# Performance work log

Hardware: AMD Instinct MI355X
Metric: run time of the kernel (lower is better)

The kernel has to match this reference:

```python
import jax, jax.numpy as jnp
import numpy as np

B = 128          # batch
T = 196          # total_patches per view (2 views -> 2*T tokens)
ENC = 1024       # encoder_embed_dim
DEC = 512        # decoder_embed_dim
V = 98           # num unmasked (visible) tokens per sample
M = 2 * T - V    # num masked tokens (294)


def setup_inputs() -> dict:
    key = jax.random.key(0)
    kx, kperm, kw, kmt, kpos, kview = jax.random.split(key, 6)
    x = jax.random.normal(kx, (B, V, ENC), jnp.float32)
    # masked_ids: unique ids per row in [0, 2T) — built from permutations
    perms = jax.vmap(jax.random.permutation, in_axes=(0, None))(
        jax.random.split(kperm, B), 2 * T)
    masked_ids = perms[:, :M].astype(jnp.int64)
    W = jax.random.normal(kw, (DEC, ENC), jnp.float32) * 0.02
    b = jnp.zeros((DEC,), jnp.float32)
    mask_token = jax.random.normal(kmt, (1, 1, DEC), jnp.float32)
    pos_embed = jax.random.normal(kpos, (1, 2 * T, DEC), jnp.float32)
    view_embed = jax.random.normal(kview, (2, DEC), jnp.float32)
    return {"x": x, "masked_ids": masked_ids, "W": W, "b": b,
            "mask_token": mask_token, "pos_embed": pos_embed,
            "view_embed": view_embed}


def reference(x, masked_ids, W, b, mask_token, pos_embed, view_embed):
    Bn = x.shape[0]
    # Linear: enc -> dec
    xp = jnp.einsum('bve,de->bvd', x, W) + b          # (B, V, DEC)
    # visible ids = sorted complement of masked_ids (vectorized, no batch loop)
    rows = jnp.arange(Bn)[:, None]
    vis_mask = jnp.ones((Bn, 2 * T), bool).at[rows, masked_ids].set(False)
    # stable argsort puts True(visible, ~mask=False) positions first, in order
    visible_ids = jnp.argsort(~vis_mask, axis=1)[:, :V]  # (B, V)
    # scatter projected visible tokens into mask-token placeholders
    base = jnp.broadcast_to(mask_token, (Bn, 2 * T, DEC))
    view = base.at[rows, visible_ids].set(xp)          # (B, 2T, DEC)
    # per-view embedding: first T tokens -> view 0, last T -> view 1
    ve = jnp.concatenate([
        jnp.broadcast_to(view_embed[0], (T, DEC)),
        jnp.broadcast_to(view_embed[1], (T, DEC))], axis=0)  # (2T, DEC)
    return view + pos_embed + ve[None, :, :]
```

## Files before the change

### kernel.cpp

```cpp
#include <hip/hip_runtime.h>

#define BATCH 128
#define VIS   98
#define TOK   196
#define TOK2  392
#define ENC   1024
#define DEC   512
#define MSK   294

#define NWB 256

#define NGEMM 784
#define NFILL 1568

typedef __bf16 bf16x8 __attribute__((ext_vector_type(8)));
typedef float  f32x4  __attribute__((ext_vector_type(4)));

__device__ __forceinline__ unsigned short f2bf(float f) {
    union { float f; unsigned u; } c; c.f = f;
    unsigned u = c.u;
    return (unsigned short)((u + 0x7fffu + ((u >> 16) & 1u)) >> 16);
}

__device__ __forceinline__ void g2lds16(const void* gptr, void* lptr) {
    __builtin_amdgcn_global_load_lds(
        (const __attribute__((address_space(1))) void*)gptr,
        (__attribute__((address_space(3))) void*)lptr, 16, 0, 0);
}

__global__ __launch_bounds__(512) void setup(const float* __restrict__ W,
                                             const int* __restrict__ mids,
                                             unsigned short* __restrict__ wbm,
                                             int* __restrict__ visids,
                                             unsigned char* __restrict__ flags) {
    int bid = blockIdx.x, tid = threadIdx.x;
    if (bid < NWB) {
        int i = bid * 512 + tid;
        float4 f = ((const float4*)W)[i];
        ushort4 o;
        o.x = f2bf(f.x); o.y = f2bf(f.y); o.z = f2bf(f.z); o.w = f2bf(f.w);
        ((ushort4*)wbm)[i] = o;
        return;
    }
    int b = bid - NWB;
    __shared__ unsigned char lf[TOK2];
    __shared__ int wtot[8];
    if (tid < TOK2) lf[tid] = 1;
    __syncthreads();
    if (tid < MSK) lf[mids[b * MSK + tid]] = 0;
    __syncthreads();
    int flag = (tid < TOK2) ? (int)lf[tid] : 0;
    unsigned long long bal = __ballot(flag != 0);
    int lane = tid & 63, wv = tid >> 6;
    int pre = __popcll(bal & ((1ull << lane) - 1ull));
    if (lane == 0) wtot[wv] = __popcll(bal);
    __syncthreads();
    int off = 0;
    for (int i = 0; i < wv; ++i) off += wtot[i];
    if (flag) visids[b * VIS + off + pre] = tid;
    if (tid < TOK2) flags[b * TOK2 + tid] = lf[tid];
}

__global__ __launch_bounds__(256, 2) void main_fused(
    const float* __restrict__ x,
    const unsigned short* __restrict__ wb,
    const float* __restrict__ bias,
    const float* __restrict__ mask_token,
    const float* __restrict__ pos,
    const float* __restrict__ ve,
    const int* __restrict__ vis,
    const unsigned char* __restrict__ flags,
    float* __restrict__ out) {
    __shared__ float Asf[2][64 * 64];
    __shared__ unsigned short Bs[2][128 * 64];
    __shared__ int rowdst[64];
    __shared__ int rowt[64];

    int bid = blockIdx.x;
    int tid = threadIdx.x;

    if (bid >= NGEMM) {
        int fb = bid - NGEMM;
        float4 m = ((const float4*)mask_token)[tid & 127];
        int g0 = fb * 4096 + tid;
        #pragma unroll 4
        for (int i = 0; i < 16; ++i) {
            int g = g0 + i * 256;
            int tok = g >> 7;
            int d4  = g & 127;
            if (flags[tok]) continue;
            int t = tok % TOK2;
            float4 p = ((const float4*)(pos + (size_t)t * DEC))[d4];
            float4 v = ((const float4*)(ve + (t >= TOK ? DEC : 0)))[d4];
            float4 r;
            r.x = m.x + p.x + v.x;
            r.y = m.y + p.y + v.y;
            r.z = m.z + p.z + v.z;
            r.w = m.w + p.w + v.w;
            ((float4*)out)[g] = r;
        }
        return;
    }

    int lane = tid & 63, w = tid >> 6;
    int l16 = lane & 15, q = lane >> 4;
    int wm = w & 1, wn = w >> 1;

    int mb, nb;
    if (bid < 768) { mb = (bid & 7) + ((bid >> 5) << 3); nb = (bid >> 3) & 3; }
    else           { int ii = bid - 768; mb = 192 + (ii & 3); nb = ii >> 2; }
    int m0 = mb * 64, n0 = nb * 128;

    if (tid < 64) {
        int gr = m0 + tid;
        int t = vis[gr];
        rowt[tid] = t;
        rowdst[tid] = (gr / VIS) * TOK2 + t;
    }

    int arow = tid >> 4;
    int cA = (tid & 15) ^ arow;
    const float* gA = x + (size_t)(m0 + arow) * ENC + cA * 4;
    int cB = (tid & 7) ^ ((tid >> 3) & 7);
    const unsigned short* gB = wb + (size_t)(n0 + (tid >> 3)) * ENC + cB * 8;

    f32x4 acc[2][4];
    #pragma unroll
    for (int i = 0; i < 2; ++i)
        #pragma unroll
        for (int j = 0; j < 4; ++j)
            acc[i][j] = (f32x4){0.f, 0.f, 0.f, 0.f};

    {
        char* lA = (char*)(&Asf[0][0]) + tid * 16;
        char* lB = (char*)(&Bs[0][0]) + tid * 16;
        #pragma unroll
        for (int tt = 0; tt < 4; ++tt)
            g2lds16(gB + (size_t)tt * 32 * ENC, lB + tt * 4096);
        #pragma unroll
        for (int tt = 0; tt < 4; ++tt)
            g2lds16(gA + (size_t)tt * 16 * ENC, lA + tt * 4096);
    }
    __syncthreads();

    for (int t = 0; t < 16; ++t) {
        int cur = t & 1;
        if (t < 15) {
            int k0 = (t + 1) << 6;
            char* lA = (char*)(&Asf[cur ^ 1][0]) + tid * 16;
            char* lB = (char*)(&Bs[cur ^ 1][0]) + tid * 16;
            #pragma unroll
            for (int tt = 0; tt < 4; ++tt)
                g2lds16(gB + (size_t)tt * 32 * ENC + k0, lB + tt * 4096);
            #pragma unroll
            for (int tt = 0; tt < 4; ++tt)
                g2lds16(gA + (size_t)tt * 16 * ENC + k0, lA + tt * 4096);
            __builtin_amdgcn_sched_barrier(0);
            asm volatile("s_waitcnt vmcnt(8)" ::: "memory");
        } else {
            __builtin_amdgcn_sched_barrier(0);
            asm volatile("s_waitcnt vmcnt(0)" ::: "memory");
        }
        __builtin_amdgcn_s_barrier();

        const char* Ab = (const char*)(&Asf[cur][0]);
        const char* Bb = (const char*)(&Bs[cur][0]);
        #pragma unroll
        for (int u = 0; u < 2; ++u) {
            int slotB = ((u * 4 + q) ^ (l16 & 7)) * 16;
            int c0 = u * 8 + q * 2;
            bf16x8 bfrag[4], afrag[2];
            #pragma unroll
            for (int j = 0; j < 4; ++j)
                bfrag[j] = *(const bf16x8*)(Bb + (wn * 64 + j * 16 + l16) * 128 + slotB);
            #pragma unroll
            for (int i = 0; i < 2; ++i) {
                const char* rowbase = Ab + (wm * 32 + i * 16 + l16) * 256;
                f32x4 lo = *(const f32x4*)(rowbase + ((c0 ^ l16) * 16));
                f32x4 hi = *(const f32x4*)(rowbase + (((c0 + 1) ^ l16) * 16));
                bf16x8 af;
                af[0] = (__bf16)lo[0]; af[1] = (__bf16)lo[1];
                af[2] = (__bf16)lo[2]; af[3] = (__bf16)lo[3];
                af[4] = (__bf16)hi[0]; af[5] = (__bf16)hi[1];
                af[6] = (__bf16)hi[2]; af[7] = (__bf16)hi[3];
                afrag[i] = af;
            }
            #pragma unroll
            for (int i = 0; i < 2; ++i)
                #pragma unroll
                for (int j = 0; j < 4; ++j)
                    acc[i][j] = __builtin_amdgcn_mfma_f32_16x16x32_bf16(afrag[i], bfrag[j], acc[i][j], 0, 0, 0);
        }
        __builtin_amdgcn_s_barrier();
    }

    #pragma unroll
    for (int j = 0; j < 4; ++j) {
        int gcol = n0 + wn * 64 + j * 16 + l16;
        float bc = bias[gcol];
        float v0 = ve[gcol];
        float v1 = ve[DEC + gcol];
        #pragma unroll
        for (int i = 0; i < 2; ++i) {
            #pragma unroll
            for (int r = 0; r < 4; ++r) {
                int rl = wm * 32 + i * 16 + q * 4 + r;
                int t = rowt[rl];
                float val = acc[i][j][r] + bc + pos[(size_t)t * DEC + gcol]
                          + (t >= TOK ? v1 : v0);
                out[(size_t)rowdst[rl] * DEC + gcol] = val;
            }
        }
    }
}

extern "C" void kernel_launch(void* const* d_in, const int* in_sizes, int n_in,
                              void* d_out, int out_size, void* d_ws, size_t ws_size,
                              hipStream_t stream) {
    (void)in_sizes; (void)n_in; (void)out_size; (void)ws_size;
    const float* x    = (const float*)d_in[0];
    const int*   mids = (const int*)d_in[1];
    const float* W    = (const float*)d_in[2];
    const float* bias = (const float*)d_in[3];
    const float* mt   = (const float*)d_in[4];
    const float* pos  = (const float*)d_in[5];
    const float* ve   = (const float*)d_in[6];
    float* out = (float*)d_out;

    unsigned short* wbm = (unsigned short*)d_ws;
    int* visids = (int*)(wbm + (size_t)DEC * ENC);
    unsigned char* flags = (unsigned char*)(visids + BATCH * VIS);

    hipLaunchKernelGGL(setup, dim3(NWB + BATCH), dim3(512), 0, stream,
                       W, mids, wbm, visids, flags);
    hipLaunchKernelGGL(main_fused, dim3(NGEMM + NFILL), dim3(256), 0, stream,
                       x, wbm, bias, mt, pos, ve, visids, flags, out);
}
```

Baseline: 189.0 us.

## Convert A tile to bf16 in registers before LDS store, raise occupancy

The A operand (x, fp32) now goes through registers. It is loaded with plain global loads, converted to bf16 once per element, and written to LDS in a swizzled bf16 layout, instead of being copied fp32 straight to LDS and converted at every fragment read. This halves A's LDS footprint and read traffic and removes redundant conversions. The smaller LDS use allows raising launch bounds to three blocks per CU. The trade-off is more registers, the loss of the direct async global-to-LDS path for A, and a full vmcnt(0) wait each iteration that may reduce load/compute overlap.

```diff
diff --git a/kernel.cpp b/kernel.cpp
--- a/kernel.cpp
+++ b/kernel.cpp
@@ -61,7 +61,7 @@
     if (tid < TOK2) flags[b * TOK2 + tid] = lf[tid];
 }
 
-__global__ __launch_bounds__(256, 2) void main_fused(
+__global__ __launch_bounds__(256, 3) void main_fused(
     const float* __restrict__ x,
     const unsigned short* __restrict__ wb,
     const float* __restrict__ bias,
@@ -71,7 +71,7 @@
     const int* __restrict__ vis,
     const unsigned char* __restrict__ flags,
     float* __restrict__ out) {
-    __shared__ float Asf[2][64 * 64];
+    __shared__ unsigned short Abf[2][64 * 64];
     __shared__ unsigned short Bs[2][128 * 64];
     __shared__ int rowdst[64];
     __shared__ int rowt[64];
@@ -118,9 +118,12 @@
         rowdst[tid] = (gr / VIS) * TOK2 + t;
     }
 
-    int arow = tid >> 4;
-    int cA = (tid & 15) ^ arow;
-    const float* gA = x + (size_t)(m0 + arow) * ENC + cA * 4;
+    int r0 = tid >> 3, sA = tid & 7;
+    int cAc = sA ^ (r0 & 7);
+    const float* gA0 = x + (size_t)(m0 + r0) * ENC + cAc * 8;
+    const float* gA1 = gA0 + (size_t)32 * ENC;
+    int aW0 = r0 * 128 + sA * 16;
+    int aW1 = aW0 + 32 * 128;
     int cB = (tid & 7) ^ ((tid >> 3) & 7);
     const unsigned short* gB = wb + (size_t)(n0 + (tid >> 3)) * ENC + cB * 8;
 
@@ -132,65 +135,72 @@
             acc[i][j] = (f32x4){0.f, 0.f, 0.f, 0.f};
 
     {
-        char* lA = (char*)(&Asf[0][0]) + tid * 16;
+        float4 p00 = ((const float4*)gA0)[0];
+        float4 p01 = ((const float4*)gA0)[1];
+        float4 p10 = ((const float4*)gA1)[0];
+        float4 p11 = ((const float4*)gA1)[1];
         char* lB = (char*)(&Bs[0][0]) + tid * 16;
         #pragma unroll
         for (int tt = 0; tt < 4; ++tt)
             g2lds16(gB + (size_t)tt * 32 * ENC, lB + tt * 4096);
-        #pragma unroll
-        for (int tt = 0; tt < 4; ++tt)
-            g2lds16(gA + (size_t)tt * 16 * ENC, lA + tt * 4096);
+        bf16x8 v0, v1;
+        v0[0] = (__bf16)p00.x; v0[1] = (__bf16)p00.y; v0[2] = (__bf16)p00.z; v0[3] = (__bf16)p00.w;
+        v0[4] = (__bf16)p01.x; v0[5] = (__bf16)p01.y; v0[6] = (__bf16)p01.z; v0[7] = (__bf16)p01.w;
+        v1[0] = (__bf16)p10.x; v1[1] = (__bf16)p10.y; v1[2] = (__bf16)p10.z; v1[3] = (__bf16)p10.w;
+        v1[4] = (__bf16)p11.x; v1[5] = (__bf16)p11.y; v1[6] = (__bf16)p11.z; v1[7] = (__bf16)p11.w;
+        *(bf16x8*)((char*)(&Abf[0][0]) + aW0) = v0;
+        *(bf16x8*)((char*)(&Abf[0][0]) + aW1) = v1;
     }
     __syncthreads();
 
     for (int t = 0; t < 16; ++t) {
-        int cur = t & 1;
+        int c = t & 1;
+        float4 n00, n01, n10, n11;
         if (t < 15) {
             int k0 = (t + 1) << 6;
-            char* lA = (char*)(&Asf[cur ^ 1][0]) + tid * 16;
-            char* lB = (char*)(&Bs[cur ^ 1][0]) + tid * 16;
+            n00 = ((const float4*)(gA0 + k0))[0];
+            n01 = ((const float4*)(gA0 + k0))[1];
+            n10 = ((const float4*)(gA1 + k0))[0];
+            n11 = ((const float4*)(gA1 + k0))[1];
+            char* lB = (char*)(&Bs[c ^ 1][0]) + tid * 16;
             #pragma unroll
             for (int tt = 0; tt < 4; ++tt)
                 g2lds16(gB + (size_t)tt * 32 * ENC + k0, lB + tt * 4096);
-            #pragma unroll
-            for (int tt = 0; tt < 4; ++tt)
-                g2lds16(gA + (size_t)tt * 16 * ENC + k0, lA + tt * 4096);
-            __builtin_amdgcn_sched_barrier(0);
-            asm volatile("s_waitcnt vmcnt(8)" ::: "memory");
-        } else {
-            __builtin_amdgcn_sched_barrier(0);
-            asm volatile("s_waitcnt vmcnt(0)" ::: "memory");
-        }
-        __builtin_amdgcn_s_barrier();
-
-        const char* Ab = (const char*)(&Asf[cur][0]);
-        const char* Bb = (const char*)(&Bs[cur][0]);
+        }
+        __builtin_amdgcn_sched_barrier(0);
+
+        const char* Ab = (const char*)(&Abf[c][0]);
+        const char* Bb = (const char*)(&Bs[c][0]);
         #pragma unroll
         for (int u = 0; u < 2; ++u) {
-            int slotB = ((u * 4 + q) ^ (l16 & 7)) * 16;
-            int c0 = u * 8 + q * 2;
+            int slot = ((u * 4 + q) ^ (l16 & 7)) * 16;
             bf16x8 bfrag[4], afrag[2];
             #pragma unroll
             for (int j = 0; j < 4; ++j)
-                bfrag[j] = *(const bf16x8*)(Bb + (wn * 64 + j * 16 + l16) * 128 + slotB);
-            #pragma unroll
-            for (int i = 0; i < 2; ++i) {
-                const char* rowbase = Ab + (wm * 32 + i * 16 + l16) * 256;
-                f32x4 lo = *(const f32x4*)(rowbase + ((c0 ^ l16) * 16));
-                f32x4 hi = *(const f32x4*)(rowbase + (((c0 + 1) ^ l16) * 16));
-                bf16x8 af;
-                af[0] = (__bf16)lo[0]; af[1] = (__bf16)lo[1];
-                af[2] = (__bf16)lo[2]; af[3] = (__bf16)lo[3];
-                af[4] = (__bf16)hi[0]; af[5] = (__bf16)hi[1];
-                af[6] = (__bf16)hi[2]; af[7] = (__bf16)hi[3];
-                afrag[i] = af;
-            }
+                bfrag[j] = *(const bf16x8*)(Bb + (wn * 64 + j * 16 + l16) * 128 + slot);
+            #pragma unroll
+            for (int i = 0; i < 2; ++i)
+                afrag[i] = *(const bf16x8*)(Ab + (wm * 32 + i * 16 + l16) * 128 + slot);
             #pragma unroll
             for (int i = 0; i < 2; ++i)
                 #pragma unroll
                 for (int j = 0; j < 4; ++j)
                     acc[i][j] = __builtin_amdgcn_mfma_f32_16x16x32_bf16(afrag[i], bfrag[j], acc[i][j], 0, 0, 0);
         }
+
+        if (t < 15) {
+            bf16x8 v0, v1;
+            v0[0] = (__bf16)n00.x; v0[1] = (__bf16)n00.y; v0[2] = (__bf16)n00.z; v0[3] = (__bf16)n00.w;
+            v0[4] = (__bf16)n01.x; v0[5] = (__bf16)n01.y; v0[6] = (__bf16)n01.z; v0[7] = (__bf16)n01.w;
+            v1[0] = (__bf16)n10.x; v1[1] = (__bf16)n10.y; v1[2] = (__bf16)n10.z; v1[3] = (__bf16)n10.w;
+            v1[4] = (__bf16)n11.x; v1[5] = (__bf16)n11.y; v1[6] = (__bf16)n11.z; v1[7] = (__bf16)n11.w;
+            *(bf16x8*)((char*)(&Abf[c ^ 1][0]) + aW0) = v0;
+            *(bf16x8*)((char*)(&Abf[c ^ 1][0]) + aW1) = v1;
+        }
+
+        __builtin_amdgcn_sched_barrier(0);
+        asm volatile("s_waitcnt vmcnt(0) lgkmcnt(0)" ::: "memory");
+        __builtin_amdgcn_sched_barrier(0);
         __builtin_amdgcn_s_barrier();
     }
 
```

After: 187.3 us. No clear change (-0.9%).
